# Performance work log

Measured on AMD Instinct MI355X. Metric: run time of the kernel, lower is better.

The kernel has to match this reference:

```python
import jax, jax.numpy as jnp
import numpy as np

SEF = 64   # skipped edge features (MLPGraphNetwork default sef)
SNF = 64   # skipped node features (MLPGraphNetwork default snf)
NR_STEPS = 3


def mlp2(x, W0, b0, W1, b1):
    # MyMLP with multI=1.0, relu hidden, linear last, no layernorm
    return jax.nn.relu(x @ W0 + b0) @ W1 + b1


def setup_inputs() -> dict:
    N, E = 50000, 800000
    nrNodeF, nrEdgeF, nrEmbed, nrTypes = 32, 3, 16, 2
    key = jax.random.key(0)
    ks = jax.random.split(key, 20)

    def w(k, fi, fo):
        # torch.normal(0,1) * (2.0 / fan_in)  (relu init in MyMLP)
        return jax.random.normal(k, (fi, fo), jnp.float32) * (2.0 / fi)

    z = lambda n: jnp.zeros((n,), jnp.float32)
    return {
        "edge_index": jax.random.randint(ks[0], (2, E), 0, N),
        "nodeFeatures": jax.random.uniform(ks[1], (N, nrNodeF), jnp.float32),
        "edgeFeatures": jax.random.normal(ks[2], (E, nrEdgeF), jnp.float32),
        "emb": jax.random.normal(ks[3], (nrTypes, nrEmbed), jnp.float32),
        "enc_n_W0": w(ks[4], nrNodeF - 1 + nrEmbed, 128), "enc_n_b0": z(128),
        "enc_n_W1": w(ks[5], 128, 128), "enc_n_b1": z(128),
        "enc_e_W0": w(ks[6], nrEdgeF, 128), "enc_e_b0": z(128),
        "enc_e_W1": w(ks[7], 128, 128), "enc_e_b1": z(128),
        "core_e_W0": w(ks[8], 192, 128), "core_e_b0": z(128),
        "core_e_W1": w(ks[9], 128, 64), "core_e_b1": z(64),
        "core_n_W0": w(ks[10], 128, 128), "core_n_b0": z(128),
        "core_n_W1": w(ks[11], 128, 64), "core_n_b1": z(64),
        "dec_W0": w(ks[12], 128, 128), "dec_b0": z(128),
        "dec_W1": w(ks[13], 128, 3), "dec_b1": z(3),
    }


def reference(edge_index, nodeFeatures, edgeFeatures, emb,
              enc_n_W0, enc_n_b0, enc_n_W1, enc_n_b1,
              enc_e_W0, enc_e_b0, enc_e_W1, enc_e_b1,
              core_e_W0, core_e_b0, core_e_W1, core_e_b1,
              core_n_W0, core_n_b0, core_n_W1, core_n_b1,
              dec_W0, dec_b0, dec_W1, dec_b1):
    N = nodeFeatures.shape[0]
    src, dst = edge_index[0], edge_index[1]  # j (source), i (target)

    # encode: embed particle type from last node feature column
    ptype = (nodeFeatures[:, -1] + 0.5).astype(jnp.int32)
    node = jnp.concatenate([nodeFeatures[:, :-1], emb[ptype]], axis=-1)
    node = mlp2(node, enc_n_W0, enc_n_b0, enc_n_W1, enc_n_b1)          # [N,128]
    edge = mlp2(edgeFeatures, enc_e_W0, enc_e_b0, enc_e_W1, enc_e_b1)  # [E,128]

    ones = jnp.ones((edge_index.shape[1],), node.dtype)
    counts = jnp.maximum(jax.ops.segment_sum(ones, dst, num_segments=N), 1.0)

    # process: shared MLPGraphNetwork applied NR_STEPS times
    for _ in range(NR_STEPS):
        einp = jnp.concatenate([edge[:, SEF:], node[dst][:, SNF:], node[src][:, SNF:]], axis=-1)  # [E,192]
        eout = mlp2(einp, core_e_W0, core_e_b0, core_e_W1, core_e_b1)  # [E,64]
        edge = jnp.concatenate([edge[:, :SEF], edge[:, SEF:] + eout], axis=-1)  # residual tail, [E,128]
        agg = jax.ops.segment_sum(edge, dst, num_segments=N) / counts[:, None]  # mean aggr, [N,128]
        ninp = jnp.concatenate([agg[:, SEF:], node[:, SNF:]], axis=-1)  # [N,128]
        nout = mlp2(ninp, core_n_W0, core_n_b0, core_n_W1, core_n_b1)  # [N,64]
        node = jnp.concatenate([node[:, :SNF], node[:, SNF:] + nout], axis=-1)  # [N,128]

    # decode
    return mlp2(node, dec_W0, dec_b0, dec_W1, dec_b1)  # [N,3]
```

## Files before the change

kernel.cpp:

```cpp
#include <hip/hip_runtime.h>
#include <cstdint>
#include <cstddef>


__global__ void k_zero(int* __restrict__ p, int n) {
    int i = blockIdx.x * 256 + threadIdx.x;
    if (i < n) p[i] = 0;
}


__global__ void k_hist(const int* __restrict__ dst, int* __restrict__ counts, int E) {
    int e = blockIdx.x * 256 + threadIdx.x;
    if (e < E) atomicAdd(&counts[dst[e]], 1);
}

__global__ __launch_bounds__(1024) void k_scan(
    const int* __restrict__ counts, int* __restrict__ row_off,
    int* __restrict__ cursor, float* __restrict__ inv_cnt, int N) {
    __shared__ int wsum[16];
    int t = threadIdx.x;
    int wave = t >> 6, lane = t & 63;
    int carry = 0;
    for (int base = 0; base < N; base += 1024) {
        int i = base + t;
        int v = (i < N) ? counts[i] : 0;
        int s = v;
        #pragma unroll
        for (int off = 1; off < 64; off <<= 1) {
            int u = __shfl_up(s, off, 64);
            if (lane >= off) s += u;
        }
        if (lane == 63) wsum[wave] = s;
        __syncthreads();
        int wpre = 0, full = 0;
        #pragma unroll
        for (int wv = 0; wv < 16; wv++) {
            int x = wsum[wv];
            full += x;
            if (wv < wave) wpre += x;
        }
        if (i < N) {
            int excl = carry + wpre + s - v;
            row_off[i] = excl;
            cursor[i]  = excl;
            inv_cnt[i] = 1.0f / (float)((v > 0) ? v : 1);
        }
        carry += full;
        __syncthreads();
    }
    if (t == 0) row_off[N] = carry;
}

__global__ void k_fill(const int* __restrict__ dst, int* __restrict__ cursor,
                       int* __restrict__ edge_list, int E) {
    int e = blockIdx.x * 256 + threadIdx.x;
    if (e < E) {
        int pos = atomicAdd(&cursor[dst[e]], 1);
        edge_list[pos] = e;
    }
}

__global__ void k_perm_idx(const int* __restrict__ elist,
                           const int* __restrict__ src, const int* __restrict__ dst,
                           int* __restrict__ src_p, int* __restrict__ dst_p, int E) {
    int i = blockIdx.x * 256 + threadIdx.x;
    if (i < E) {
        int e = elist[i];
        src_p[i] = src[e];
        dst_p[i] = dst[e];
    }
}


__global__ void k_embW(const float* __restrict__ emb, const float* __restrict__ W0,
                       const float* __restrict__ b0, float* __restrict__ embW) {
    int c = threadIdx.x;
    #pragma unroll
    for (int p = 0; p < 2; p++) {
        float acc = b0[c];
        #pragma unroll
        for (int k = 0; k < 16; k++)
            acc = fmaf(emb[p * 16 + k], W0[(31 + k) * 128 + c], acc);
        embW[p * 128 + c] = acc;
    }
}


__device__ __forceinline__ void g1_accum32(
    const float4* __restrict__ a4, int kk4,
    const float* __restrict__ W, int cbase, float* __restrict__ h) {
    #pragma clang loop unroll(disable)
    for (int kk = 0; kk < kk4; kk++) {
        float4 a = a4[kk];
        const float* wr = W + (size_t)kk * 4 * 128 + cbase;
        const float4* w0 = reinterpret_cast<const float4*>(wr);
        const float4* w1 = reinterpret_cast<const float4*>(wr + 128);
        const float4* w2 = reinterpret_cast<const float4*>(wr + 256);
        const float4* w3 = reinterpret_cast<const float4*>(wr + 384);
        #pragma unroll
        for (int cg = 0; cg < 8; cg++) {
            float4 p = w0[cg], q = w1[cg], r = w2[cg], s = w3[cg];
            h[cg*4+0] = fmaf(a.w, s.x, fmaf(a.z, r.x, fmaf(a.y, q.x, fmaf(a.x, p.x, h[cg*4+0]))));
            h[cg*4+1] = fmaf(a.w, s.y, fmaf(a.z, r.y, fmaf(a.y, q.y, fmaf(a.x, p.y, h[cg*4+1]))));
            h[cg*4+2] = fmaf(a.w, s.z, fmaf(a.z, r.z, fmaf(a.y, q.z, fmaf(a.x, p.z, h[cg*4+2]))));
            h[cg*4+3] = fmaf(a.w, s.w, fmaf(a.z, r.w, fmaf(a.y, q.w, fmaf(a.x, p.w, h[cg*4+3]))));
        }
    }
}

__device__ __forceinline__ void g1_tail3(
    float x, float y, float z, const float* __restrict__ W, int cbase,
    float* __restrict__ h) {
    const float4* w0 = reinterpret_cast<const float4*>(W + cbase);
    const float4* w1 = reinterpret_cast<const float4*>(W + 128 + cbase);
    const float4* w2 = reinterpret_cast<const float4*>(W + 256 + cbase);
    #pragma unroll
    for (int cg = 0; cg < 8; cg++) {
        float4 p = w0[cg], q = w1[cg], r = w2[cg];
        h[cg*4+0] = fmaf(z, r.x, fmaf(y, q.x, fmaf(x, p.x, h[cg*4+0])));
        h[cg*4+1] = fmaf(z, r.y, fmaf(y, q.y, fmaf(x, p.y, h[cg*4+1])));
        h[cg*4+2] = fmaf(z, r.z, fmaf(y, q.z, fmaf(x, p.z, h[cg*4+2])));
        h[cg*4+3] = fmaf(z, r.w, fmaf(y, q.w, fmaf(x, p.w, h[cg*4+3])));
    }
}

__device__ __forceinline__ void g2_accum64(
    float* __restrict__ sb, const float* __restrict__ hc,
    const float* __restrict__ W1, int kbase, int rs, float* __restrict__ o) {
    int t = threadIdx.x;
    #pragma unroll
    for (int k = 0; k < 32; k++) sb[k * 256 + t] = hc[k];
    __syncthreads();
    #pragma clang loop unroll(disable)
    for (int k = 0; k < 32; k++) {
        float hk = sb[k * 256 + t];
        const float4* w = reinterpret_cast<const float4*>(W1 + (size_t)(kbase + k) * rs);
        #pragma unroll
        for (int cg = 0; cg < 16; cg++) {
            float4 wv = w[cg];
            o[cg*4+0] = fmaf(hk, wv.x, o[cg*4+0]);
            o[cg*4+1] = fmaf(hk, wv.y, o[cg*4+1]);
            o[cg*4+2] = fmaf(hk, wv.z, o[cg*4+2]);
            o[cg*4+3] = fmaf(hk, wv.w, o[cg*4+3]);
        }
    }
    __syncthreads();
}


__global__ __launch_bounds__(256, 2) void k_enc_node_tail(
    const float* __restrict__ nodeF, const float* __restrict__ embW,
    const float* __restrict__ W0, const float* __restrict__ W1,
    const float* __restrict__ b1, float* __restrict__ nodeT, int N) {
    __shared__ float sb[32 * 256];
    int n = blockIdx.x * 256 + threadIdx.x;
    bool valid = n < N;
    int nc = valid ? n : N - 1;
    const float4* nf4 = reinterpret_cast<const float4*>(nodeF + (size_t)nc * 32);
    float4 v7 = nf4[7];
    int p = (int)(v7.w + 0.5f);
    const float4* ew = reinterpret_cast<const float4*>(embW + p * 128);

    float o[64];
    const float4* bv = reinterpret_cast<const float4*>(b1 + 64);
    #pragma unroll
    for (int i = 0; i < 16; i++) {
        float4 b = bv[i];
        o[4*i+0] = b.x; o[4*i+1] = b.y; o[4*i+2] = b.z; o[4*i+3] = b.w;
    }
    #pragma unroll
    for (int ch = 0; ch < 4; ch++) {
        int cbase = ch * 32;
        float h[32];
        #pragma unroll
        for (int i = 0; i < 8; i++) {
            float4 u = ew[ch*8 + i];
            h[4*i+0] = u.x; h[4*i+1] = u.y; h[4*i+2] = u.z; h[4*i+3] = u.w;
        }
        g1_accum32(nf4, 7, W0, cbase, h);
        g1_tail3(v7.x, v7.y, v7.z, W0 + 28*128, cbase, h);
        #pragma unroll
        for (int i = 0; i < 32; i++) h[i] = fmaxf(h[i], 0.0f);
        g2_accum64(sb, h, W1 + 64, cbase, 128, o);
    }
    if (valid) {
        float4* out4 = reinterpret_cast<float4*>(nodeT + (size_t)n * 64);
        #pragma unroll
        for (int i = 0; i < 16; i++)
            out4[i] = make_float4(o[4*i], o[4*i+1], o[4*i+2], o[4*i+3]);
    }
}


__global__ __launch_bounds__(256, 2) void k_enc_edge(
    const float* __restrict__ edgeF, const int* __restrict__ perm, int usePerm,
    const float* __restrict__ W0, const float* __restrict__ b0,
    const float* __restrict__ W1, const float* __restrict__ b1,
    float* __restrict__ edgeT, int E) {
    __shared__ float sb[32 * 256];
    int e = blockIdx.x * 256 + threadIdx.x;
    bool valid = e < E;
    int ec = valid ? e : E - 1;
    int e2 = usePerm ? perm[ec] : ec;
    float x0 = edgeF[(size_t)e2 * 3 + 0];
    float x1 = edgeF[(size_t)e2 * 3 + 1];
    float x2 = edgeF[(size_t)e2 * 3 + 2];

    float o[64];
    const float4* bv = reinterpret_cast<const float4*>(b1 + 64);
    #pragma unroll
    for (int i = 0; i < 16; i++) {
        float4 b = bv[i];
        o[4*i+0] = b.x; o[4*i+1] = b.y; o[4*i+2] = b.z; o[4*i+3] = b.w;
    }
    #pragma unroll
    for (int ch = 0; ch < 4; ch++) {
        int cbase = ch * 32;
        float h[32];
        const float4* b0v = reinterpret_cast<const float4*>(b0 + cbase);
        #pragma unroll
        for (int i = 0; i < 8; i++) {
            float4 b = b0v[i];
            h[4*i+0] = b.x; h[4*i+1] = b.y; h[4*i+2] = b.z; h[4*i+3] = b.w;
        }
        g1_tail3(x0, x1, x2, W0, cbase, h);
        #pragma unroll
        for (int i = 0; i < 32; i++) h[i] = fmaxf(h[i], 0.0f);
        g2_accum64(sb, h, W1 + 64, cbase, 128, o);
    }
    if (valid) {
        float4* out4 = reinterpret_cast<float4*>(edgeT + (size_t)e * 64);
        #pragma unroll
        for (int i = 0; i < 16; i++)
            out4[i] = make_float4(o[4*i], o[4*i+1], o[4*i+2], o[4*i+3]);
    }
}


__global__ __launch_bounds__(256, 4) void k_node_pre_d(
    const float* __restrict__ nodeT, const float* __restrict__ W0,
    const float* __restrict__ b0, float* __restrict__ Pd, int N) {
    int n = blockIdx.x * 256 + threadIdx.x;
    bool valid = n < N;
    int nc = valid ? n : N - 1;
    const float4* a4 = reinterpret_cast<const float4*>(nodeT + (size_t)nc * 64);

    #pragma unroll
    for (int ch = 0; ch < 4; ch++) {
        int cbase = ch * 32;
        float h[32];
        const float4* b0v = reinterpret_cast<const float4*>(b0 + cbase);
        #pragma unroll
        for (int i = 0; i < 8; i++) {
            float4 b = b0v[i];
            h[4*i+0] = b.x; h[4*i+1] = b.y; h[4*i+2] = b.z; h[4*i+3] = b.w;
        }
        g1_accum32(a4, 16, W0 + 64*128, cbase, h);
        if (valid) {
            float4* o4 = reinterpret_cast<float4*>(Pd + (size_t)n * 128 + cbase);
            #pragma unroll
            for (int i = 0; i < 8; i++)
                o4[i] = make_float4(h[4*i], h[4*i+1], h[4*i+2], h[4*i+3]);
        }
    }
}


__global__ __launch_bounds__(256, 3) void k_edge_core_T(
    float* __restrict__ edgeT, const float* __restrict__ Pd,
    const float* __restrict__ nodeT,
    const int* __restrict__ srcI, const int* __restrict__ dstI,
    const float* __restrict__ W0, const float* __restrict__ W1,
    const float* __restrict__ b1, int E) {
    __shared__ float Abuf[2 * 64 * 65];
    __shared__ float Wbuf[32 * 132];

    int t = threadIdx.x;
    int base = blockIdx.x * 64;

    {
        int i = t >> 2, q = t & 3;
        int e = base + i; int ec = (e < E) ? e : E - 1;
        const float4* er = reinterpret_cast<const float4*>(edgeT + (size_t)ec * 64 + q * 16);
        int s = srcI[ec];
        const float4* sr = reinterpret_cast<const float4*>(nodeT + (size_t)s * 64 + q * 16);
        float* ae = Abuf + i * 65 + q * 16;
        float* as = Abuf + 64 * 65 + i * 65 + q * 16;
        #pragma unroll
        for (int j4 = 0; j4 < 4; j4++) {
            float4 v = er[j4];
            ae[j4*4+0]=v.x; ae[j4*4+1]=v.y; ae[j4*4+2]=v.z; ae[j4*4+3]=v.w;
            float4 w = sr[j4];
            as[j4*4+0]=w.x; as[j4*4+1]=w.y; as[j4*4+2]=w.z; as[j4*4+3]=w.w;
        }
    }

    int eg = t & 15, cg = t >> 4;
    float c1[4][8];
    #pragma unroll
    for (int ie = 0; ie < 4; ie++) {
        int e = base + eg * 4 + ie; int ec = (e < E) ? e : E - 1;
        int d = dstI[ec];
        const float4* pr = reinterpret_cast<const float4*>(Pd + (size_t)d * 128 + cg * 8);
        float4 p0 = pr[0], p1 = pr[1];
        c1[ie][0]=p0.x; c1[ie][1]=p0.y; c1[ie][2]=p0.z; c1[ie][3]=p0.w;
        c1[ie][4]=p1.x; c1[ie][5]=p1.y; c1[ie][6]=p1.z; c1[ie][7]=p1.w;
    }

    #pragma clang loop unroll(disable)
    for (int phase = 0; phase < 4; phase++) {
        int wrow = (phase < 2) ? phase * 32 : 128 + (phase - 2) * 32;
        const float* Asrc = Abuf + ((phase < 2) ? 0 : 64 * 65);
        int koff = (phase & 1) * 32;
        __syncthreads();
        {
            int r = t >> 3, cb = t & 7;
            const float4* wr = reinterpret_cast<const float4*>(
                W0 + (size_t)(wrow + r) * 128 + cb * 16);
            float* wd = Wbuf + r * 132 + cb * 16;
            #pragma unroll
            for (int j4 = 0; j4 < 4; j4++) {
                float4 v = wr[j4];
                wd[j4*4+0]=v.x; wd[j4*4+1]=v.y; wd[j4*4+2]=v.z; wd[j4*4+3]=v.w;
            }
        }
        __syncthreads();
        #pragma clang loop unroll_count(4)
        for (int k = 0; k < 32; k++) {
            float a0 = Asrc[(eg*4+0)*65 + koff + k];
            float a1 = Asrc[(eg*4+1)*65 + koff + k];
            float a2 = Asrc[(eg*4+2)*65 + koff + k];
            float a3 = Asrc[(eg*4+3)*65 + koff + k];
            const float* wr = Wbuf + k * 132 + cg * 8;
            float4 bq0 = *reinterpret_cast<const float4*>(wr);
            float4 bq1 = *reinterpret_cast<const float4*>(wr + 4);
            float bb[8] = {bq0.x,bq0.y,bq0.z,bq0.w,bq1.x,bq1.y,bq1.z,bq1.w};
            #pragma unroll
            for (int jc = 0; jc < 8; jc++) {
                c1[0][jc] = fmaf(a0, bb[jc], c1[0][jc]);
                c1[1][jc] = fmaf(a1, bb[jc], c1[1][jc]);
                c1[2][jc] = fmaf(a2, bb[jc], c1[2][jc]);
                c1[3][jc] = fmaf(a3, bb[jc], c1[3][jc]);
            }
        }
    }

    __syncthreads();
    float* H = Abuf;
    #pragma unroll
    for (int ie = 0; ie < 4; ie++)
        #pragma unroll
        for (int jc = 0; jc < 8; jc++)
            H[(cg*8 + jc) * 65 + eg*4 + ie] = fmaxf(c1[ie][jc], 0.0f);

    int eg2 = t & 15, cg2 = t >> 4;
    float c2[4][4];
    {
        float4 bv = *reinterpret_cast<const float4*>(b1 + cg2 * 4);
        #pragma unroll
        for (int ie = 0; ie < 4; ie++) {
            c2[ie][0]=bv.x; c2[ie][1]=bv.y; c2[ie][2]=bv.z; c2[ie][3]=bv.w;
        }
    }
    #pragma clang loop unroll(disable)
    for (int phase = 0; phase < 4; phase++) {
        __syncthreads();
        {
            int r = t >> 3, cb = t & 7;
            const float4* wr = reinterpret_cast<const float4*>(
                W1 + (size_t)(phase * 32 + r) * 64 + cb * 8);
            float* wd = Wbuf + r * 68 + cb * 8;
            float4 v0 = wr[0], v1 = wr[1];
            wd[0]=v0.x; wd[1]=v0.y; wd[2]=v0.z; wd[3]=v0.w;
            wd[4]=v1.x; wd[5]=v1.y; wd[6]=v1.z; wd[7]=v1.w;
        }
        __syncthreads();
        #pragma clang loop unroll_count(4)
        for (int k = 0; k < 32; k++) {
            int c = phase * 32 + k;
            float a0 = H[c*65 + eg2*4 + 0];
            float a1 = H[c*65 + eg2*4 + 1];
            float a2 = H[c*65 + eg2*4 + 2];
            float a3 = H[c*65 + eg2*4 + 3];
            float4 b4 = *reinterpret_cast<const float4*>(Wbuf + k * 68 + cg2 * 4);
            float bb[4] = {b4.x, b4.y, b4.z, b4.w};
            #pragma unroll
            for (int jc = 0; jc < 4; jc++) {
                c2[0][jc] = fmaf(a0, bb[jc], c2[0][jc]);
                c2[1][jc] = fmaf(a1, bb[jc], c2[1][jc]);
                c2[2][jc] = fmaf(a2, bb[jc], c2[2][jc]);
                c2[3][jc] = fmaf(a3, bb[jc], c2[3][jc]);
            }
        }
    }

    #pragma unroll
    for (int ie = 0; ie < 4; ie++) {
        int e = base + eg2 * 4 + ie;
        if (e < E) {
            float4* er = reinterpret_cast<float4*>(edgeT + (size_t)e * 64 + cg2 * 4);
            float4 old = *er;
            old.x += c2[ie][0]; old.y += c2[ie][1];
            old.z += c2[ie][2]; old.w += c2[ie][3];
            *er = old;
        }
    }
}


__global__ __launch_bounds__(256, 2) void k_edge_core_B(
    float* __restrict__ edgeT, const float* __restrict__ nodeT,
    const int* __restrict__ src, const int* __restrict__ dst,
    const float* __restrict__ W0, const float* __restrict__ b0,
    const float* __restrict__ W1, const float* __restrict__ b1, int E) {
    __shared__ float sb[32 * 256];
    int e = blockIdx.x * 256 + threadIdx.x;
    bool valid = e < E;
    int ec = valid ? e : E - 1;
    int d = dst[ec], s = src[ec];
    const float4* a4 = reinterpret_cast<const float4*>(edgeT + (size_t)ec * 64);
    const float4* d4 = reinterpret_cast<const float4*>(nodeT + (size_t)d * 64);
    const float4* s4 = reinterpret_cast<const float4*>(nodeT + (size_t)s * 64);

    float o[64];
    const float4* bv = reinterpret_cast<const float4*>(b1);
    #pragma unroll
    for (int i = 0; i < 16; i++) {
        float4 b = bv[i];
        o[4*i+0] = b.x; o[4*i+1] = b.y; o[4*i+2] = b.z; o[4*i+3] = b.w;
    }
    #pragma unroll
    for (int ch = 0; ch < 4; ch++) {
        int cbase = ch * 32;
        float h[32];
        const float4* b0v = reinterpret_cast<const float4*>(b0 + cbase);
        #pragma unroll
        for (int i = 0; i < 8; i++) {
            float4 b = b0v[i];
            h[4*i+0] = b.x; h[4*i+1] = b.y; h[4*i+2] = b.z; h[4*i+3] = b.w;
        }
        g1_accum32(a4, 16, W0, cbase, h);
        g1_accum32(d4, 16, W0 + 64*128, cbase, h);
        g1_accum32(s4, 16, W0 + 128*128, cbase, h);
        #pragma unroll
        for (int i = 0; i < 32; i++) h[i] = fmaxf(h[i], 0.0f);
        g2_accum64(sb, h, W1, cbase, 64, o);
    }
    if (valid) {
        float4* eo4 = reinterpret_cast<float4*>(edgeT + (size_t)e * 64);
        #pragma unroll
        for (int i = 0; i < 16; i++) {
            float4 t = a4[i];
            t.x += o[4*i+0]; t.y += o[4*i+1];
            t.z += o[4*i+2]; t.w += o[4*i+3];
            eo4[i] = t;
        }
    }
}


__global__ __launch_bounds__(256) void k_agg_csr(
    const float* __restrict__ edgeT, const int* __restrict__ row_off,
    const float* __restrict__ inv_cnt, float* __restrict__ aggT, int N) {
    int n = blockIdx.x * 4 + (threadIdx.x >> 6);
    int lane = threadIdx.x & 63;
    if (n >= N) return;
    int beg = row_off[n], end = row_off[n + 1];
    double s = 0.0;
    for (int idx = beg; idx < end; idx++)
        s += (double)edgeT[(size_t)idx * 64 + lane];
    aggT[(size_t)n * 64 + lane] = (float)(s * (double)inv_cnt[n]);
}

__global__ __launch_bounds__(256) void k_agg_gather(
    const float* __restrict__ edgeT, const int* __restrict__ row_off,
    const int* __restrict__ edge_list, const float* __restrict__ inv_cnt,
    float* __restrict__ aggT, int N) {
    int n = blockIdx.x * 4 + (threadIdx.x >> 6);
    int lane = threadIdx.x & 63;
    if (n >= N) return;
    int beg = row_off[n], end = row_off[n + 1];
    double s = 0.0;
    for (int idx = beg; idx < end; idx++) {
        int e = edge_list[idx];
        s += (double)edgeT[(size_t)e * 64 + lane];
    }
    aggT[(size_t)n * 64 + lane] = (float)(s * (double)inv_cnt[n]);
}


__global__ __launch_bounds__(256, 2) void k_node_core(
    const float* __restrict__ aggT, float* __restrict__ nodeT,
    const float* __restrict__ W0, const float* __restrict__ b0,
    const float* __restrict__ W1, const float* __restrict__ b1, int N) {
    __shared__ float sb[32 * 256];
    int n = blockIdx.x * 256 + threadIdx.x;
    bool valid = n < N;
    int nc = valid ? n : N - 1;
    const float4* g4 = reinterpret_cast<const float4*>(aggT + (size_t)nc * 64);
    const float4* t4 = reinterpret_cast<const float4*>(nodeT + (size_t)nc * 64);

    float o[64];
    const float4* bv = reinterpret_cast<const float4*>(b1);
    #pragma unroll
    for (int i = 0; i < 16; i++) {
        float4 b = bv[i];
        o[4*i+0] = b.x; o[4*i+1] = b.y; o[4*i+2] = b.z; o[4*i+3] = b.w;
    }
    #pragma unroll
    for (int ch = 0; ch < 4; ch++) {
        int cbase = ch * 32;
        float h[32];
        const float4* b0v = reinterpret_cast<const float4*>(b0 + cbase);
        #pragma unroll
        for (int i = 0; i < 8; i++) {
            float4 b = b0v[i];
            h[4*i+0] = b.x; h[4*i+1] = b.y; h[4*i+2] = b.z; h[4*i+3] = b.w;
        }
        g1_accum32(g4, 16, W0, cbase, h);
        g1_accum32(t4, 16, W0 + 64*128, cbase, h);
        #pragma unroll
        for (int i = 0; i < 32; i++) h[i] = fmaxf(h[i], 0.0f);
        g2_accum64(sb, h, W1, cbase, 64, o);
    }
    if (valid) {
        float4* nt4 = reinterpret_cast<float4*>(nodeT + (size_t)n * 64);
        #pragma unroll
        for (int i = 0; i < 16; i++) {
            float4 t = t4[i];
            t.x += o[4*i+0]; t.y += o[4*i+1];
            t.z += o[4*i+2]; t.w += o[4*i+3];
            nt4[i] = t;
        }
    }
}


__global__ __launch_bounds__(256, 2) void k_decode(
    const float* __restrict__ nodeF, const float* __restrict__ embW,
    const float* __restrict__ encW0, const float* __restrict__ encW1,
    const float* __restrict__ encb1, const float* __restrict__ nodeT,
    const float* __restrict__ W0, const float* __restrict__ b0,
    const float* __restrict__ W1, const float* __restrict__ b1,
    float* __restrict__ out, int N) {
    __shared__ float sb[64 * 256];
    int t = threadIdx.x;
    int n = blockIdx.x * 256 + t;
    bool valid = n < N;
    int nc = valid ? n : N - 1;
    const float4* nf4 = reinterpret_cast<const float4*>(nodeF + (size_t)nc * 32);
    const float4* t4  = reinterpret_cast<const float4*>(nodeT + (size_t)nc * 64);
    float4 v7 = nf4[7];
    int p = (int)(v7.w + 0.5f);
    const float4* ew = reinterpret_cast<const float4*>(embW + p * 128);

    float head[64];
    const float4* ebv = reinterpret_cast<const float4*>(encb1);
    #pragma unroll
    for (int i = 0; i < 16; i++) {
        float4 b = ebv[i];
        head[4*i+0] = b.x; head[4*i+1] = b.y; head[4*i+2] = b.z; head[4*i+3] = b.w;
    }
    #pragma unroll
    for (int ch = 0; ch < 4; ch++) {
        int cbase = ch * 32;
        float h[32];
        #pragma unroll
        for (int i = 0; i < 8; i++) {
            float4 u = ew[ch*8 + i];
            h[4*i+0] = u.x; h[4*i+1] = u.y; h[4*i+2] = u.z; h[4*i+3] = u.w;
        }
        g1_accum32(nf4, 7, encW0, cbase, h);
        g1_tail3(v7.x, v7.y, v7.z, encW0 + 28*128, cbase, h);
        #pragma unroll
        for (int i = 0; i < 32; i++) h[i] = fmaxf(h[i], 0.0f);
        g2_accum64(sb, h, encW1, cbase, 128, head);
    }

    #pragma unroll
    for (int k = 0; k < 64; k++) sb[k * 256 + t] = head[k];
    __syncthreads();

    float h2[128];
    #pragma unroll
    for (int ch = 0; ch < 4; ch++) {
        int cbase = ch * 32;
        float* hc = &h2[ch * 32];
        const float4* b0v = reinterpret_cast<const float4*>(b0 + cbase);
        #pragma unroll
        for (int i = 0; i < 8; i++) {
            float4 b = b0v[i];
            hc[4*i+0] = b.x; hc[4*i+1] = b.y; hc[4*i+2] = b.z; hc[4*i+3] = b.w;
        }
        #pragma clang loop unroll(disable)
        for (int k = 0; k < 64; k++) {
            float hk = sb[k * 256 + t];
            const float4* w = reinterpret_cast<const float4*>(W0 + (size_t)k * 128 + cbase);
            #pragma unroll
            for (int cg = 0; cg < 8; cg++) {
                float4 wv = w[cg];
                hc[cg*4+0] = fmaf(hk, wv.x, hc[cg*4+0]);
                hc[cg*4+1] = fmaf(hk, wv.y, hc[cg*4+1]);
                hc[cg*4+2] = fmaf(hk, wv.z, hc[cg*4+2]);
                hc[cg*4+3] = fmaf(hk, wv.w, hc[cg*4+3]);
            }
        }
        g1_accum32(t4, 16, W0 + 64*128, cbase, hc);
    }
    __syncthreads();

    float o0 = b1[0], o1 = b1[1], o2 = b1[2];
    #pragma unroll
    for (int ch = 0; ch < 4; ch++) {
        int kb = ch * 32;
        #pragma unroll
        for (int k = 0; k < 32; k++) sb[k * 256 + t] = fmaxf(h2[kb + k], 0.0f);
        __syncthreads();
        #pragma clang loop unroll(disable)
        for (int k = 0; k < 32; k++) {
            float hk = sb[k * 256 + t];
            const float* w = W1 + (size_t)(kb + k) * 3;
            o0 = fmaf(hk, w[0], o0);
            o1 = fmaf(hk, w[1], o1);
            o2 = fmaf(hk, w[2], o2);
        }
        __syncthreads();
    }
    if (valid) {
        out[(size_t)n * 3 + 0] = o0;
        out[(size_t)n * 3 + 1] = o1;
        out[(size_t)n * 3 + 2] = o2;
    }
}


extern "C" void kernel_launch(void* const* d_in, const int* in_sizes, int n_in,
                              void* d_out, int out_size, void* d_ws, size_t ws_size,
                              hipStream_t stream) {
    const int*   edge_index = (const int*)  d_in[0];
    const float* nodeF      = (const float*)d_in[1];
    const float* edgeF      = (const float*)d_in[2];
    const float* emb        = (const float*)d_in[3];
    const float* enc_n_W0   = (const float*)d_in[4];
    const float* enc_n_b0   = (const float*)d_in[5];
    const float* enc_n_W1   = (const float*)d_in[6];
    const float* enc_n_b1   = (const float*)d_in[7];
    const float* enc_e_W0   = (const float*)d_in[8];
    const float* enc_e_b0   = (const float*)d_in[9];
    const float* enc_e_W1   = (const float*)d_in[10];
    const float* enc_e_b1   = (const float*)d_in[11];
    const float* core_e_W0  = (const float*)d_in[12];
    const float* core_e_b0  = (const float*)d_in[13];
    const float* core_e_W1  = (const float*)d_in[14];
    const float* core_e_b1  = (const float*)d_in[15];
    const float* core_n_W0  = (const float*)d_in[16];
    const float* core_n_b0  = (const float*)d_in[17];
    const float* core_n_W1  = (const float*)d_in[18];
    const float* core_n_b1  = (const float*)d_in[19];
    const float* dec_W0     = (const float*)d_in[20];
    const float* dec_b0     = (const float*)d_in[21];
    const float* dec_W1     = (const float*)d_in[22];
    const float* dec_b1     = (const float*)d_in[23];
    (void)n_in; (void)out_size;

    const int E = in_sizes[0] / 2;
    const int N = in_sizes[1] / 32;
    const int* src = edge_index;
    const int* dst = edge_index + E;

    auto al = [](size_t x) { return (x + 255) & ~(size_t)255; };
    const size_t szEdgeT = al((size_t)E * 64 * 4);
    const size_t szNodeT = al((size_t)N * 64 * 4);
    const size_t szP     = al((size_t)N * 128 * 4);
    const size_t szAgg   = al((size_t)N * 64 * 4);
    const size_t szElist = al((size_t)E * 4);
    const size_t szN4    = al((size_t)N * 4);
    const size_t szRow   = al((size_t)(N + 1) * 4);
    const size_t szEmbW  = al(2 * 128 * 4);
    const size_t base = szEdgeT + szNodeT + szElist + szRow + 3 * szN4 + szEmbW;
    const size_t needCSR = base + 2 * szElist + szP;
    const size_t needAp  = base + szP;
    const int plan = (ws_size >= needCSR) ? 0 : (ws_size >= needAp) ? 1 : 2;

    char* ws = (char*)d_ws;
    size_t off = 0;
    auto carve = [&](size_t bytes) -> char* { char* p = ws + off; off += bytes; return p; };
    float* edgeT   = (float*)carve(szEdgeT);
    float* nodeT   = (float*)carve(szNodeT);
    int*   elist   = (int*)  carve(szElist);
    int*   row_off = (int*)  carve(szRow);
    int*   counts  = (int*)  carve(szN4);
    int*   cursor  = (int*)  carve(szN4);
    float* inv_cnt = (float*)carve(szN4);
    float* embW    = (float*)carve(szEmbW);
    int *src_p = nullptr, *dst_p = nullptr;
    float *Pd = nullptr, *aggT = nullptr;
    if (plan == 0) {
        src_p = (int*)carve(szElist);
        dst_p = (int*)carve(szElist);
        Pd = (float*)carve(szP); aggT = Pd;
    } else if (plan == 1) {
        Pd = (float*)carve(szP); aggT = Pd;
    } else {
        aggT = (float*)carve(szAgg);
    }

    int blkE = (E + 255) / 256;
    int blkN = (N + 255) / 256;
    int blkT = (E + 63) / 64;

    k_zero<<<(N + 255) / 256, 256, 0, stream>>>(counts, N);
    k_hist<<<blkE, 256, 0, stream>>>(dst, counts, E);
    k_scan<<<1, 1024, 0, stream>>>(counts, row_off, cursor, inv_cnt, N);
    k_fill<<<blkE, 256, 0, stream>>>(dst, cursor, elist, E);
    if (plan == 0)
        k_perm_idx<<<blkE, 256, 0, stream>>>(elist, src, dst, src_p, dst_p, E);

    k_embW<<<1, 128, 0, stream>>>(emb, enc_n_W0, enc_n_b0, embW);
    k_enc_node_tail<<<blkN, 256, 0, stream>>>(nodeF, embW, enc_n_W0, enc_n_W1,
                                              enc_n_b1, nodeT, N);
    k_enc_edge<<<blkE, 256, 0, stream>>>(edgeF, elist, (plan == 0) ? 1 : 0,
                                         enc_e_W0, enc_e_b0, enc_e_W1, enc_e_b1,
                                         edgeT, E);

    for (int step = 0; step < 3; step++) {
        if (plan == 0) {
            k_node_pre_d<<<blkN, 256, 0, stream>>>(nodeT, core_e_W0, core_e_b0, Pd, N);
            k_edge_core_T<<<blkT, 256, 0, stream>>>(edgeT, Pd, nodeT, src_p, dst_p,
                                                    core_e_W0, core_e_W1, core_e_b1, E);
            k_agg_csr<<<(N + 3) / 4, 256, 0, stream>>>(edgeT, row_off, inv_cnt, aggT, N);
        } else if (plan == 1) {
            k_node_pre_d<<<blkN, 256, 0, stream>>>(nodeT, core_e_W0, core_e_b0, Pd, N);
            k_edge_core_T<<<blkT, 256, 0, stream>>>(edgeT, Pd, nodeT, src, dst,
                                                    core_e_W0, core_e_W1, core_e_b1, E);
            k_agg_gather<<<(N + 3) / 4, 256, 0, stream>>>(edgeT, row_off, elist,
                                                          inv_cnt, aggT, N);
        } else {
            k_edge_core_B<<<blkE, 256, 0, stream>>>(edgeT, nodeT, src, dst,
                                                    core_e_W0, core_e_b0,
                                                    core_e_W1, core_e_b1, E);
            k_agg_gather<<<(N + 3) / 4, 256, 0, stream>>>(edgeT, row_off, elist,
                                                          inv_cnt, aggT, N);
        }
        k_node_core<<<blkN, 256, 0, stream>>>(aggT, nodeT, core_n_W0, core_n_b0,
                                              core_n_W1, core_n_b1, N);
    }
    k_decode<<<blkN, 256, 0, stream>>>(nodeF, embW, enc_n_W0, enc_n_W1, enc_n_b1,
                                       nodeT, dec_W0, dec_b0, dec_W1, dec_b1,
                                       (float*)d_out, N);
}
```

Baseline: 3.162 ms.

## Rewrite edge encoder as block-tiled 64-edge GEMM with shared hidden buffer

The edge encoder previously used one thread per edge, each running a full 128x64 second-layer product with weights staged through shared memory. It now processes 64 edges per block with register-tiled outer products: a 4x8 tile for the first layer, hidden activations stored transposed in shared memory, and a 4x4 tile for the second layer, with W1 loaded in chunks. The aim is more weight reuse across edges and fewer registers per thread, so occupancy can rise to 3 blocks per SM. The edge core kernel also changes its edge-to-thread mapping from contiguous to strided (eg+16*ie), likely to reduce LDS bank conflicts.

```diff
diff --git a/kernel.cpp b/kernel.cpp
--- a/kernel.cpp
+++ b/kernel.cpp
@@ -192,47 +192,103 @@
 }
 
 
-__global__ __launch_bounds__(256, 2) void k_enc_edge(
+__global__ __launch_bounds__(256, 3) void k_enc_edge_T(
     const float* __restrict__ edgeF, const int* __restrict__ perm, int usePerm,
     const float* __restrict__ W0, const float* __restrict__ b0,
     const float* __restrict__ W1, const float* __restrict__ b1,
     float* __restrict__ edgeT, int E) {
-    __shared__ float sb[32 * 256];
-    int e = blockIdx.x * 256 + threadIdx.x;
-    bool valid = e < E;
-    int ec = valid ? e : E - 1;
-    int e2 = usePerm ? perm[ec] : ec;
-    float x0 = edgeF[(size_t)e2 * 3 + 0];
-    float x1 = edgeF[(size_t)e2 * 3 + 1];
-    float x2 = edgeF[(size_t)e2 * 3 + 2];
-
-    float o[64];
-    const float4* bv = reinterpret_cast<const float4*>(b1 + 64);
-    #pragma unroll
-    for (int i = 0; i < 16; i++) {
-        float4 b = bv[i];
-        o[4*i+0] = b.x; o[4*i+1] = b.y; o[4*i+2] = b.z; o[4*i+3] = b.w;
-    }
-    #pragma unroll
-    for (int ch = 0; ch < 4; ch++) {
-        int cbase = ch * 32;
-        float h[32];
-        const float4* b0v = reinterpret_cast<const float4*>(b0 + cbase);
-        #pragma unroll
-        for (int i = 0; i < 8; i++) {
-            float4 b = b0v[i];
-            h[4*i+0] = b.x; h[4*i+1] = b.y; h[4*i+2] = b.z; h[4*i+3] = b.w;
-        }
-        g1_tail3(x0, x1, x2, W0, cbase, h);
-        #pragma unroll
-        for (int i = 0; i < 32; i++) h[i] = fmaxf(h[i], 0.0f);
-        g2_accum64(sb, h, W1 + 64, cbase, 128, o);
-    }
-    if (valid) {
-        float4* out4 = reinterpret_cast<float4*>(edgeT + (size_t)e * 64);
-        #pragma unroll
-        for (int i = 0; i < 16; i++)
-            out4[i] = make_float4(o[4*i], o[4*i+1], o[4*i+2], o[4*i+3]);
+    __shared__ float H[128 * 65];
+    __shared__ float Wbuf[32 * 68];
+    __shared__ float Xs[64 * 4];
+
+    int t = threadIdx.x;
+    int base = blockIdx.x * 64;
+
+    if (t < 192) {
+        int i = t / 3, j = t - i * 3;
+        int e = base + i; int ec = (e < E) ? e : E - 1;
+        int e2 = usePerm ? perm[ec] : ec;
+        Xs[i * 4 + j] = edgeF[(size_t)e2 * 3 + j];
+    }
+    __syncthreads();
+
+    int eg = t & 15, cg = t >> 4;
+    float c1[4][8];
+    {
+        float4 b0a = *reinterpret_cast<const float4*>(b0 + cg * 8);
+        float4 b0b = *reinterpret_cast<const float4*>(b0 + cg * 8 + 4);
+        float bb[8] = {b0a.x,b0a.y,b0a.z,b0a.w,b0b.x,b0b.y,b0b.z,b0b.w};
+        #pragma unroll
+        for (int ie = 0; ie < 4; ie++)
+            #pragma unroll
+            for (int jc = 0; jc < 8; jc++) c1[ie][jc] = bb[jc];
+    }
+    #pragma unroll
+    for (int k = 0; k < 3; k++) {
+        float4 wa = *reinterpret_cast<const float4*>(W0 + k * 128 + cg * 8);
+        float4 wb = *reinterpret_cast<const float4*>(W0 + k * 128 + cg * 8 + 4);
+        float ww[8] = {wa.x,wa.y,wa.z,wa.w,wb.x,wb.y,wb.z,wb.w};
+        #pragma unroll
+        for (int ie = 0; ie < 4; ie++) {
+            float a = Xs[(eg + 16 * ie) * 4 + k];
+            #pragma unroll
+            for (int jc = 0; jc < 8; jc++)
+                c1[ie][jc] = fmaf(a, ww[jc], c1[ie][jc]);
+        }
+    }
+    #pragma unroll
+    for (int ie = 0; ie < 4; ie++)
+        #pragma unroll
+        for (int jc = 0; jc < 8; jc++)
+            H[(cg * 8 + jc) * 65 + eg + 16 * ie] = fmaxf(c1[ie][jc], 0.0f);
+
+    int eg2 = t & 15, cg2 = t >> 4;
+    float c2[4][4];
+    {
+        float4 bv = *reinterpret_cast<const float4*>(b1 + 64 + cg2 * 4);
+        #pragma unroll
+        for (int ie = 0; ie < 4; ie++) {
+            c2[ie][0]=bv.x; c2[ie][1]=bv.y; c2[ie][2]=bv.z; c2[ie][3]=bv.w;
+        }
+    }
+    #pragma clang loop unroll(disable)
+    for (int phase = 0; phase < 4; phase++) {
+        __syncthreads();
+        {
+            int r = t >> 3, cb = t & 7;
+            const float4* wr = reinterpret_cast<const float4*>(
+                W1 + (size_t)(phase * 32 + r) * 128 + 64 + cb * 8);
+            float* wd = Wbuf + r * 68 + cb * 8;
+            float4 v0 = wr[0], v1 = wr[1];
+            wd[0]=v0.x; wd[1]=v0.y; wd[2]=v0.z; wd[3]=v0.w;
+            wd[4]=v1.x; wd[5]=v1.y; wd[6]=v1.z; wd[7]=v1.w;
+        }
+        __syncthreads();
+        #pragma clang loop unroll_count(4)
+        for (int k = 0; k < 32; k++) {
+            int c = phase * 32 + k;
+            float a0 = H[c*65 + eg2*4 + 0];
+            float a1 = H[c*65 + eg2*4 + 1];
+            float a2 = H[c*65 + eg2*4 + 2];
+            float a3 = H[c*65 + eg2*4 + 3];
+            float4 b4 = *reinterpret_cast<const float4*>(Wbuf + k * 68 + cg2 * 4);
+            float bb[4] = {b4.x, b4.y, b4.z, b4.w};
+            #pragma unroll
+            for (int jc = 0; jc < 4; jc++) {
+                c2[0][jc] = fmaf(a0, bb[jc], c2[0][jc]);
+                c2[1][jc] = fmaf(a1, bb[jc], c2[1][jc]);
+                c2[2][jc] = fmaf(a2, bb[jc], c2[2][jc]);
+                c2[3][jc] = fmaf(a3, bb[jc], c2[3][jc]);
+            }
+        }
+    }
+    #pragma unroll
+    for (int ie = 0; ie < 4; ie++) {
+        int e = base + eg2 * 4 + ie;
+        if (e < E) {
+            *reinterpret_cast<float4*>(edgeT + (size_t)e * 64 + cg2 * 4) =
+                make_float4(c2[ie][0], c2[ie][1], c2[ie][2], c2[ie][3]);
+        }
     }
 }
 
@@ -299,7 +355,7 @@
     float c1[4][8];
     #pragma unroll
     for (int ie = 0; ie < 4; ie++) {
-        int e = base + eg * 4 + ie; int ec = (e < E) ? e : E - 1;
+        int e = base + eg + 16 * ie; int ec = (e < E) ? e : E - 1;
         int d = dstI[ec];
         const float4* pr = reinterpret_cast<const float4*>(Pd + (size_t)d * 128 + cg * 8);
         float4 p0 = pr[0], p1 = pr[1];
@@ -327,10 +383,10 @@
         __syncthreads();
         #pragma clang loop unroll_count(4)
         for (int k = 0; k < 32; k++) {
-            float a0 = Asrc[(eg*4+0)*65 + koff + k];
-            float a1 = Asrc[(eg*4+1)*65 + koff + k];
-            float a2 = Asrc[(eg*4+2)*65 + koff + k];
-            float a3 = Asrc[(eg*4+3)*65 + koff + k];
+            float a0 = Asrc[(eg + 16*0)*65 + koff + k];
+            float a1 = Asrc[(eg + 16*1)*65 + koff + k];
+            float a2 = Asrc[(eg + 16*2)*65 + koff + k];
+            float a3 = Asrc[(eg + 16*3)*65 + koff + k];
             const float* wr = Wbuf + k * 132 + cg * 8;
             float4 bq0 = *reinterpret_cast<const float4*>(wr);
             float4 bq1 = *reinterpret_cast<const float4*>(wr + 4);
@@ -351,7 +407,7 @@
     for (int ie = 0; ie < 4; ie++)
         #pragma unroll
         for (int jc = 0; jc < 8; jc++)
-            H[(cg*8 + jc) * 65 + eg*4 + ie] = fmaxf(c1[ie][jc], 0.0f);
+            H[(cg*8 + jc) * 65 + eg + 16*ie] = fmaxf(c1[ie][jc], 0.0f);
 
     int eg2 = t & 15, cg2 = t >> 4;
     float c2[4][4];
@@ -719,9 +775,9 @@
     k_embW<<<1, 128, 0, stream>>>(emb, enc_n_W0, enc_n_b0, embW);
     k_enc_node_tail<<<blkN, 256, 0, stream>>>(nodeF, embW, enc_n_W0, enc_n_W1,
                                               enc_n_b1, nodeT, N);
-    k_enc_edge<<<blkE, 256, 0, stream>>>(edgeF, elist, (plan == 0) ? 1 : 0,
-                                         enc_e_W0, enc_e_b0, enc_e_W1, enc_e_b1,
-                                         edgeT, E);
+    k_enc_edge_T<<<blkT, 256, 0, stream>>>(edgeF, elist, (plan == 0) ? 1 : 0,
+                                           enc_e_W0, enc_e_b0, enc_e_W1, enc_e_b1,
+                                           edgeT, E);
 
     for (int step = 0; step < 3; step++) {
         if (plan == 0) {
```

Result: faster. 3.063 ms (-3.1%).
